# Kernel tuning notes

Measured on AMD Instinct MI355X. Metric: run time of the kernel, lower is better.

Reference implementation:

```python
import jax, jax.numpy as jnp
import numpy as np

# CaMoE_Block MoE dispatch/combine reference.
# Assumptions (undefined submodules in source): RWKV7_TimeMix/att residual omitted
# (h = ln2(x) directly); SparseRWKVFFN experts modeled as RWKV channel-mix FFNs
# y = relu(h @ W1)^2 @ W2; the LinearTransformerExpert (last expert) uses the same
# FFN form with recon_loss = 0; per-expert confidence head conf_e = sigmoid(h @ wc_e + bc_e).
# Faithful parts: winner selection, winning-bid lookup, straight-through scale
# factor conf / (stop_grad(conf) + 1e-6), per-expert compute, scatter-combine, residual.

B, T, C = 4, 2048, 1024
E = 5            # num_rwkv_experts + 1
H = 4 * C        # FFN hidden
LN_EPS = 1e-5


def setup_inputs() -> dict:
    key = jax.random.key(0)
    ks = jax.random.split(key, 8)
    x = jax.random.normal(ks[0], (B, T, C), dtype=jnp.float32)
    winners = jax.random.randint(ks[1], (B, T), 0, E)
    gamma = jnp.ones((C,), jnp.float32)
    beta = jnp.zeros((C,), jnp.float32)
    w1 = jax.random.normal(ks[2], (E, C, H), jnp.float32) * (1.0 / np.sqrt(C))
    w2 = jax.random.normal(ks[3], (E, H, C), jnp.float32) * (1.0 / np.sqrt(H))
    wc = jax.random.normal(ks[4], (E, C), jnp.float32) * (1.0 / np.sqrt(C))
    bc = jnp.zeros((E,), jnp.float32)
    return {"x": x, "winners": winners, "gamma": gamma, "beta": beta,
            "w1": w1, "w2": w2, "wc": wc, "bc": bc}


def _layernorm(x, gamma, beta):
    mu = jnp.mean(x, axis=-1, keepdims=True)
    var = jnp.mean(jnp.square(x - mu), axis=-1, keepdims=True)
    return (x - mu) * jax.lax.rsqrt(var + LN_EPS) * gamma + beta


def reference(x, winners, gamma, beta, w1, w2, wc, bc):
    b, t, c = x.shape
    e = w1.shape[0]
    h = _layernorm(x, gamma, beta)
    hf = h.reshape(-1, c)                     # [N, C]
    win = winners.reshape(-1)                 # [N]

    # per-expert confidences (bids)
    conf = jax.nn.sigmoid(hf @ wc.T + bc)     # [N, E]
    winning_bids = jnp.take_along_axis(conf, win[:, None], axis=1)  # [N, 1]
    scale = winning_bids / (jax.lax.stop_gradient(winning_bids) + 1e-6)

    # dense all-expert FFN (squared-ReLU channel mix), then top-1 select
    k = jnp.square(jax.nn.relu(jnp.einsum('nc,ech->enh', hf, w1)))  # [E, N, H]
    y = jnp.einsum('enh,ehc->enc', k, w2)                            # [E, N, C]
    sel = jax.nn.one_hot(win, e, dtype=y.dtype)                      # [N, E]
    expert_out = jnp.einsum('ne,enc->nc', sel, y)                    # scatter-combine

    out = (expert_out * scale).reshape(b, t, c)
    return x + out
```

## Files before the change

### kernel.cpp

```cpp
#include <hip/hip_runtime.h>
#include <hip/hip_bf16.h>
#include <stdint.h>

#define N_TOK 8192
#define C_DIM 1024
#define H_DIM 4096
#define E_NUM 5
#define LN_EPS 1e-5f
#define NT_MAX 69
#define N_PAD (NT_MAX * 128)

typedef __hip_bfloat16 bf16;
using s8v = __attribute__((ext_vector_type(8))) short;
using f4v = __attribute__((ext_vector_type(4))) float;

__device__ __forceinline__ void async_ld16(const bf16* g, bf16* l) {
    __builtin_amdgcn_global_load_lds(
        (const __attribute__((address_space(1))) void*)g,
        (__attribute__((address_space(3))) void*)l,
        16, 0, 0);
}

__global__ void init_meta_kernel(int* meta) {
    if (threadIdx.x < 16) meta[threadIdx.x] = 0;
}

__global__ __launch_bounds__(256) void count_kernel(
    const int* __restrict__ win, int* __restrict__ meta)
{
    __shared__ int c[E_NUM];
    if (threadIdx.x < E_NUM) c[threadIdx.x] = 0;
    __syncthreads();
    int n = blockIdx.x * 256 + threadIdx.x;
    atomicAdd(&c[win[n]], 1);
    __syncthreads();
    if (threadIdx.x < E_NUM) atomicAdd(&meta[threadIdx.x], c[threadIdx.x]);
}

__global__ void scan_kernel(int* meta) {
    if (threadIdx.x == 0) {
        int off = 0;
        for (int e = 0; e < E_NUM; ++e) {
            meta[5 + e] = off;
            off += (meta[e] + 127) & ~127;
            meta[11 + e] = 0;
        }
        meta[10] = off;
        int ti = 0;
        for (int e = 0; e < E_NUM; ++e) {
            int tiles = (meta[e] + 127) >> 7;
            for (int j = 0; j < tiles; ++j) meta[16 + ti++] = e;
        }
        for (; ti < NT_MAX; ++ti) meta[16 + ti] = -1;
    }
}

__global__ __launch_bounds__(256) void scatter_kernel(
    const int* __restrict__ win, int* __restrict__ meta,
    int* __restrict__ idx, int* __restrict__ pos)
{
    __shared__ int c[E_NUM];
    __shared__ int base[E_NUM];
    if (threadIdx.x < E_NUM) c[threadIdx.x] = 0;
    __syncthreads();
    int n = blockIdx.x * 256 + threadIdx.x;
    int e = win[n];
    int lr = atomicAdd(&c[e], 1);
    __syncthreads();
    if (threadIdx.x < E_NUM)
        base[threadIdx.x] = atomicAdd(&meta[11 + threadIdx.x], c[threadIdx.x]);
    __syncthreads();
    int p = meta[5 + e] + base[e] + lr;
    idx[p] = n;
    pos[n] = p;
}

__global__ __launch_bounds__(256) void ln_conf_kernel(
    const float* __restrict__ x, const int* __restrict__ win,
    const float* __restrict__ gamma, const float* __restrict__ beta,
    const float* __restrict__ wc, const float* __restrict__ bc,
    const int* __restrict__ pos,
    bf16* __restrict__ hbuf, float* __restrict__ scl)
{
    int n = blockIdx.x;
    int t = threadIdx.x;
    const float* xr = x + (size_t)n * C_DIM;
    float v[4];
    float s = 0.f, ss = 0.f;
#pragma unroll
    for (int i = 0; i < 4; ++i) {
        v[i] = xr[t + i * 256];
        s += v[i];
        ss += v[i] * v[i];
    }
#pragma unroll
    for (int off = 32; off > 0; off >>= 1) {
        s  += __shfl_down(s, off);
        ss += __shfl_down(ss, off);
    }
    __shared__ float red[8];
    __shared__ float mu_s, rv_s;
    int wave = t >> 6, lane = t & 63;
    if (lane == 0) { red[wave] = s; red[4 + wave] = ss; }
    __syncthreads();
    if (t == 0) {
        float S  = red[0] + red[1] + red[2] + red[3];
        float SS = red[4] + red[5] + red[6] + red[7];
        float mu = S * (1.f / C_DIM);
        float var = SS * (1.f / C_DIM) - mu * mu;
        mu_s = mu;
        rv_s = rsqrtf(var + LN_EPS);
    }
    __syncthreads();
    float mu = mu_s, rv = rv_s;
    int e = win[n];
    int p = pos[n];
    const float* wce = wc + (size_t)e * C_DIM;
    float dot = 0.f;
#pragma unroll
    for (int i = 0; i < 4; ++i) {
        int ci = t + i * 256;
        float hv = (v[i] - mu) * rv * gamma[ci] + beta[ci];
        hbuf[(size_t)p * C_DIM + ci] = (bf16)hv;
        dot += hv * wce[ci];
    }
#pragma unroll
    for (int off = 32; off > 0; off >>= 1) dot += __shfl_down(dot, off);
    if (lane == 0) red[wave] = dot;
    __syncthreads();
    if (t == 0) {
        float z = red[0] + red[1] + red[2] + red[3] + bc[e];
        float conf = 1.f / (1.f + expf(-z));
        scl[p] = conf / (conf + 1e-6f);
    }
}

__global__ __launch_bounds__(256) void transpose_cvt_kernel(
    const float* __restrict__ src, bf16* __restrict__ dst, int R, int S)
{
    __shared__ float tile[64][65];
    size_t ebase = (size_t)blockIdx.z * (size_t)R * (size_t)S;
    int s0 = blockIdx.x * 64;
    int r0 = blockIdx.y * 64;
    int t = threadIdx.x;
    int lr = t >> 4;
    int lc = (t & 15) * 4;
#pragma unroll
    for (int i = 0; i < 4; ++i) {
        int r = lr + i * 16;
        float4 v = *(const float4*)(src + ebase + (size_t)(r0 + r) * S + s0 + lc);
        tile[r][lc + 0] = v.x;
        tile[r][lc + 1] = v.y;
        tile[r][lc + 2] = v.z;
        tile[r][lc + 3] = v.w;
    }
    __syncthreads();
    int sc = t >> 2;
#pragma unroll
    for (int p = 0; p < 2; ++p) {
        int ch = (t & 3) + p * 4;
        bf16 vals[8];
#pragma unroll
        for (int j = 0; j < 8; ++j)
            vals[j] = (bf16)tile[ch * 8 + j][sc];
        *(s8v*)(dst + ebase + (size_t)(s0 + sc) * R + r0 + ch * 8) = *(s8v*)vals;
    }
}


__global__ __launch_bounds__(256) void gemm1_kernel(
    const bf16* __restrict__ hbuf, const bf16* __restrict__ w1t,
    const int* __restrict__ meta, bf16* __restrict__ ks)
{
    const int GX = H_DIM / 128;
    const int NWG = GX * NT_MAX;
    int d = blockIdx.y * GX + blockIdx.x;
    int w = (d & 7) * (NWG >> 3) + (d >> 3);
    int bx = w & (GX - 1);
    int ti = w / GX;
    int e = meta[16 + ti];
    if (e < 0) return;

    int base_p = meta[5 + e];
    int cnt = meta[e];
    int m0 = ti * 128 - base_p;
    int n0 = bx * 128;

    __shared__ __align__(16) bf16 As[128 * 32];
    __shared__ __align__(16) bf16 Bs[128 * 32];

    int t = threadIdx.x;
    int lane = t & 63;
    int wv = t >> 6;
    int wr = wv >> 1, wcol = wv & 1;

    int i0 = (t & 7) ^ ((t >> 3) & 7);
    int srow = 2 * (t >> 3) + (i0 >> 2);
    int schk = i0 & 3;

    int r1 = min(m0 + srow, cnt - 1);
    int r2 = min(m0 + 64 + srow, cnt - 1);
    const bf16* ga1 = hbuf + (size_t)(base_p + r1) * C_DIM + schk * 8;
    const bf16* ga2 = hbuf + (size_t)(base_p + r2) * C_DIM + schk * 8;
    const bf16* wbase = w1t + (size_t)e * H_DIM * C_DIM;
    const bf16* gb1 = wbase + (size_t)(n0 + srow) * C_DIM + schk * 8;
    const bf16* gb2 = wbase + (size_t)(n0 + 64 + srow) * C_DIM + schk * 8;

    bf16* la1 = As + t * 8;
    bf16* la2 = As + 2048 + t * 8;
    bf16* lb1 = Bs + t * 8;
    bf16* lb2 = Bs + 2048 + t * 8;

    int kq = lane >> 4;
    int rhalf = (lane & 15) >> 1;
    int ifrag = ((lane & 1) << 2) | kq;
    int foff = rhalf * 64 + (ifrag ^ rhalf) * 8;
    const bf16* Af = As + wr * 2048 + foff;
    const bf16* Bf = Bs + wcol * 2048 + foff;

    f4v acc[4][4];
    f4v zero = {0.f, 0.f, 0.f, 0.f};
#pragma unroll
    for (int i = 0; i < 4; ++i)
#pragma unroll
        for (int j = 0; j < 4; ++j) acc[i][j] = zero;

    for (int kb = 0; kb < C_DIM / 32; ++kb) {
        __syncthreads();
        async_ld16(ga1, la1); ga1 += 32;
        async_ld16(ga2, la2); ga2 += 32;
        async_ld16(gb1, lb1); gb1 += 32;
        async_ld16(gb2, lb2); gb2 += 32;
        __syncthreads();
        s8v af[4], bfv[4];
#pragma unroll
        for (int mi = 0; mi < 4; ++mi)
            af[mi] = *(const s8v*)(Af + mi * 512);
#pragma unroll
        for (int ni = 0; ni < 4; ++ni)
            bfv[ni] = *(const s8v*)(Bf + ni * 512);
#pragma unroll
        for (int mi = 0; mi < 4; ++mi)
#pragma unroll
            for (int ni = 0; ni < 4; ++ni)
                acc[mi][ni] = __builtin_amdgcn_mfma_f32_16x16x32_bf16(af[mi], bfv[ni], acc[mi][ni], 0, 0, 0);
    }

#pragma unroll
    for (int mi = 0; mi < 4; ++mi) {
#pragma unroll
        for (int r = 0; r < 4; ++r) {
            int row_local = wr * 64 + mi * 16 + ((lane >> 4) << 2) + r;
            int gm = m0 + row_local;
            if (gm < cnt) {
                size_t p = (size_t)(base_p + gm);
#pragma unroll
                for (int ni = 0; ni < 4; ++ni) {
                    int col = n0 + wcol * 64 + ni * 16 + (lane & 15);
                    float v = acc[mi][ni][r];
                    float rl = fmaxf(v, 0.f);
                    ks[p * H_DIM + col] = (bf16)(rl * rl);
                }
            }
        }
    }
}

__global__ __launch_bounds__(256) void gemm2_kernel(
    const bf16* __restrict__ ks, const bf16* __restrict__ w2t,
    const int* __restrict__ idx, const int* __restrict__ meta,
    const float* __restrict__ x, const float* __restrict__ scl,
    float* __restrict__ out)
{
    const int GX = C_DIM / 128;
    const int NWG = GX * NT_MAX;
    int d = blockIdx.y * GX + blockIdx.x;
    int w = (d & 7) * (NWG >> 3) + (d >> 3);
    int bx = w & (GX - 1);
    int ti = w / GX;
    int e = meta[16 + ti];
    if (e < 0) return;

    int base_p = meta[5 + e];
    int cnt = meta[e];
    int m0 = ti * 128 - base_p;
    int n0 = bx * 128;

    __shared__ __align__(16) bf16 As[3][128 * 32];
    __shared__ __align__(16) bf16 Bs[3][128 * 32];

    int t = threadIdx.x;
    int lane = t & 63;
    int wv = t >> 6;
    int wr = wv >> 1, wcol = wv & 1;

    int i0 = (t & 7) ^ ((t >> 3) & 7);
    int srow = 2 * (t >> 3) + (i0 >> 2);
    int schk = i0 & 3;

    int r1 = min(m0 + srow, cnt - 1);
    int r2 = min(m0 + 64 + srow, cnt - 1);
    const bf16* ga1 = ks + (size_t)(base_p + r1) * H_DIM + schk * 8;
    const bf16* ga2 = ks + (size_t)(base_p + r2) * H_DIM + schk * 8;
    const bf16* wbase = w2t + (size_t)e * C_DIM * H_DIM;
    const bf16* gb1 = wbase + (size_t)(n0 + srow) * H_DIM + schk * 8;
    const bf16* gb2 = wbase + (size_t)(n0 + 64 + srow) * H_DIM + schk * 8;

    int lo1 = t * 8;
    int lo2 = 2048 + t * 8;

    int kq = lane >> 4;
    int rhalf = (lane & 15) >> 1;
    int ifrag = ((lane & 1) << 2) | kq;
    int foff = rhalf * 64 + (ifrag ^ rhalf) * 8;
    int aoff = wr * 2048 + foff;
    int boff = wcol * 2048 + foff;

    f4v acc[4][4];
    f4v zero = {0.f, 0.f, 0.f, 0.f};
#pragma unroll
    for (int i = 0; i < 4; ++i)
#pragma unroll
        for (int j = 0; j < 4; ++j) acc[i][j] = zero;

    const int nk = H_DIM / 32;

#pragma unroll
    for (int pt = 0; pt < 2; ++pt) {
        async_ld16(ga1, &As[pt][lo1]); ga1 += 32;
        async_ld16(ga2, &As[pt][lo2]); ga2 += 32;
        async_ld16(gb1, &Bs[pt][lo1]); gb1 += 32;
        async_ld16(gb2, &Bs[pt][lo2]); gb2 += 32;
    }

    int cur = 0, st = 2;
    for (int kb = 0; kb < nk; ++kb) {
        if (kb < nk - 2) {
            async_ld16(ga1, &As[st][lo1]); ga1 += 32;
            async_ld16(ga2, &As[st][lo2]); ga2 += 32;
            async_ld16(gb1, &Bs[st][lo1]); gb1 += 32;
            async_ld16(gb2, &Bs[st][lo2]); gb2 += 32;
            asm volatile("s_waitcnt vmcnt(8)" ::: "memory");
        } else if (kb == nk - 2) {
            asm volatile("s_waitcnt vmcnt(4)" ::: "memory");
        } else {
            asm volatile("s_waitcnt vmcnt(0)" ::: "memory");
        }
        __builtin_amdgcn_s_barrier();

        const bf16* Ac = &As[cur][0];
        const bf16* Bc = &Bs[cur][0];
        s8v af[4], bfv[4];
#pragma unroll
        for (int mi = 0; mi < 4; ++mi)
            af[mi] = *(const s8v*)(Ac + aoff + mi * 512);
#pragma unroll
        for (int ni = 0; ni < 4; ++ni)
            bfv[ni] = *(const s8v*)(Bc + boff + ni * 512);
#pragma unroll
        for (int mi = 0; mi < 4; ++mi)
#pragma unroll
            for (int ni = 0; ni < 4; ++ni)
                acc[mi][ni] = __builtin_amdgcn_mfma_f32_16x16x32_bf16(af[mi], bfv[ni], acc[mi][ni], 0, 0, 0);

        asm volatile("s_waitcnt lgkmcnt(0)" ::: "memory");
        __builtin_amdgcn_s_barrier();
        cur = (cur == 2) ? 0 : cur + 1;
        st  = (st  == 2) ? 0 : st  + 1;
    }

#pragma unroll
    for (int mi = 0; mi < 4; ++mi) {
        int tok[4];
        float sclv[4];
#pragma unroll
        for (int r = 0; r < 4; ++r) {
            int row_local = wr * 64 + mi * 16 + ((lane >> 4) << 2) + r;
            int gm = m0 + row_local;
            if (gm < cnt) {
                tok[r] = idx[base_p + gm];
                sclv[r] = scl[base_p + gm];
            } else {
                tok[r] = -1;
                sclv[r] = 0.f;
            }
        }
#pragma unroll
        for (int ni = 0; ni < 4; ++ni) {
            int col = n0 + wcol * 64 + ni * 16 + (lane & 15);
#pragma unroll
            for (int r = 0; r < 4; ++r) {
                if (tok[r] >= 0) {
                    size_t o = (size_t)tok[r] * C_DIM + col;
                    out[o] = x[o] + acc[mi][ni][r] * sclv[r];
                }
            }
        }
    }
}

extern "C" void kernel_launch(void* const* d_in, const int* in_sizes, int n_in,
                              void* d_out, int out_size, void* d_ws, size_t ws_size,
                              hipStream_t stream) {
    const float* x     = (const float*)d_in[0];
    const int*   win   = (const int*)d_in[1];
    const float* gamma = (const float*)d_in[2];
    const float* beta  = (const float*)d_in[3];
    const float* w1    = (const float*)d_in[4];
    const float* w2    = (const float*)d_in[5];
    const float* wc    = (const float*)d_in[6];
    const float* bc    = (const float*)d_in[7];
    float* out = (float*)d_out;

    char* ws = (char*)d_ws;
    size_t o = 0;
    bf16* w1t  = (bf16*)(ws + o); o += (size_t)E_NUM * H_DIM * C_DIM * 2;
    bf16* w2t  = (bf16*)(ws + o); o += (size_t)E_NUM * C_DIM * H_DIM * 2;
    bf16* hbuf = (bf16*)(ws + o); o += (size_t)N_PAD * C_DIM * 2;
    bf16* ks   = (bf16*)(ws + o); o += (size_t)N_PAD * H_DIM * 2;
    float* scl = (float*)(ws + o); o += (size_t)N_PAD * 4;
    int* idx   = (int*)(ws + o);   o += (size_t)N_PAD * 4;
    int* pos   = (int*)(ws + o);   o += (size_t)N_TOK * 4;
    int* meta  = (int*)(ws + o);   o += 512;

    hipLaunchKernelGGL(init_meta_kernel, dim3(1), dim3(64), 0, stream, meta);
    hipLaunchKernelGGL(count_kernel, dim3(N_TOK / 256), dim3(256), 0, stream, win, meta);
    hipLaunchKernelGGL(scan_kernel, dim3(1), dim3(64), 0, stream, meta);
    hipLaunchKernelGGL(scatter_kernel, dim3(N_TOK / 256), dim3(256), 0, stream, win, meta, idx, pos);
    hipLaunchKernelGGL(transpose_cvt_kernel, dim3(H_DIM / 64, C_DIM / 64, E_NUM), dim3(256), 0, stream,
                       w1, w1t, C_DIM, H_DIM);
    hipLaunchKernelGGL(transpose_cvt_kernel, dim3(C_DIM / 64, H_DIM / 64, E_NUM), dim3(256), 0, stream,
                       w2, w2t, H_DIM, C_DIM);
    hipLaunchKernelGGL(ln_conf_kernel, dim3(N_TOK), dim3(256), 0, stream,
                       x, win, gamma, beta, wc, bc, pos, hbuf, scl);
    hipLaunchKernelGGL(gemm1_kernel, dim3(H_DIM / 128, NT_MAX), dim3(256), 0, stream,
                       hbuf, w1t, meta, ks);
    hipLaunchKernelGGL(gemm2_kernel, dim3(C_DIM / 128, NT_MAX), dim3(256), 0, stream,
                       ks, w2t, idx, meta, x, scl, out);
}
```

Baseline: 443.7 us.

## Pipeline gemm1 with triple-buffered async loads and deepen gemm2 to four stages

The first expert GEMM drops its single-buffer load/sync loop and uses the same triple-buffered async global-to-LDS pipeline as the second GEMM, with vmcnt-based waits. The second GEMM goes from three to four stages, keeping more loads in flight. Both kernels raise wave priority around the MFMA block, and the transpose kernel changes its write-thread mapping so that consecutive threads write adjacent 16-byte chunks of one row. The cost is more LDS per workgroup, which may reduce occupancy.

```diff
diff --git a/kernel.cpp b/kernel.cpp
--- a/kernel.cpp
+++ b/kernel.cpp
@@ -155,10 +155,11 @@
         tile[r][lc + 3] = v.w;
     }
     __syncthreads();
-    int sc = t >> 2;
+    int ch = t & 7;
+    int scb = t >> 3;
 #pragma unroll
     for (int p = 0; p < 2; ++p) {
-        int ch = (t & 3) + p * 4;
+        int sc = scb + p * 32;
         bf16 vals[8];
 #pragma unroll
         for (int j = 0; j < 8; ++j)
@@ -186,8 +187,8 @@
     int m0 = ti * 128 - base_p;
     int n0 = bx * 128;
 
-    __shared__ __align__(16) bf16 As[128 * 32];
-    __shared__ __align__(16) bf16 Bs[128 * 32];
+    __shared__ __align__(16) bf16 As[3][128 * 32];
+    __shared__ __align__(16) bf16 Bs[3][128 * 32];
 
     int t = threadIdx.x;
     int lane = t & 63;
@@ -206,106 +207,6 @@
     const bf16* gb1 = wbase + (size_t)(n0 + srow) * C_DIM + schk * 8;
     const bf16* gb2 = wbase + (size_t)(n0 + 64 + srow) * C_DIM + schk * 8;
 
-    bf16* la1 = As + t * 8;
-    bf16* la2 = As + 2048 + t * 8;
-    bf16* lb1 = Bs + t * 8;
-    bf16* lb2 = Bs + 2048 + t * 8;
-
-    int kq = lane >> 4;
-    int rhalf = (lane & 15) >> 1;
-    int ifrag = ((lane & 1) << 2) | kq;
-    int foff = rhalf * 64 + (ifrag ^ rhalf) * 8;
-    const bf16* Af = As + wr * 2048 + foff;
-    const bf16* Bf = Bs + wcol * 2048 + foff;
-
-    f4v acc[4][4];
-    f4v zero = {0.f, 0.f, 0.f, 0.f};
-#pragma unroll
-    for (int i = 0; i < 4; ++i)
-#pragma unroll
-        for (int j = 0; j < 4; ++j) acc[i][j] = zero;
-
-    for (int kb = 0; kb < C_DIM / 32; ++kb) {
-        __syncthreads();
-        async_ld16(ga1, la1); ga1 += 32;
-        async_ld16(ga2, la2); ga2 += 32;
-        async_ld16(gb1, lb1); gb1 += 32;
-        async_ld16(gb2, lb2); gb2 += 32;
-        __syncthreads();
-        s8v af[4], bfv[4];
-#pragma unroll
-        for (int mi = 0; mi < 4; ++mi)
-            af[mi] = *(const s8v*)(Af + mi * 512);
-#pragma unroll
-        for (int ni = 0; ni < 4; ++ni)
-            bfv[ni] = *(const s8v*)(Bf + ni * 512);
-#pragma unroll
-        for (int mi = 0; mi < 4; ++mi)
-#pragma unroll
-            for (int ni = 0; ni < 4; ++ni)
-                acc[mi][ni] = __builtin_amdgcn_mfma_f32_16x16x32_bf16(af[mi], bfv[ni], acc[mi][ni], 0, 0, 0);
-    }
-
-#pragma unroll
-    for (int mi = 0; mi < 4; ++mi) {
-#pragma unroll
-        for (int r = 0; r < 4; ++r) {
-            int row_local = wr * 64 + mi * 16 + ((lane >> 4) << 2) + r;
-            int gm = m0 + row_local;
-            if (gm < cnt) {
-                size_t p = (size_t)(base_p + gm);
-#pragma unroll
-                for (int ni = 0; ni < 4; ++ni) {
-                    int col = n0 + wcol * 64 + ni * 16 + (lane & 15);
-                    float v = acc[mi][ni][r];
-                    float rl = fmaxf(v, 0.f);
-                    ks[p * H_DIM + col] = (bf16)(rl * rl);
-                }
-            }
-        }
-    }
-}
-
-__global__ __launch_bounds__(256) void gemm2_kernel(
-    const bf16* __restrict__ ks, const bf16* __restrict__ w2t,
-    const int* __restrict__ idx, const int* __restrict__ meta,
-    const float* __restrict__ x, const float* __restrict__ scl,
-    float* __restrict__ out)
-{
-    const int GX = C_DIM / 128;
-    const int NWG = GX * NT_MAX;
-    int d = blockIdx.y * GX + blockIdx.x;
-    int w = (d & 7) * (NWG >> 3) + (d >> 3);
-    int bx = w & (GX - 1);
-    int ti = w / GX;
-    int e = meta[16 + ti];
-    if (e < 0) return;
-
-    int base_p = meta[5 + e];
-    int cnt = meta[e];
-    int m0 = ti * 128 - base_p;
-    int n0 = bx * 128;
-
-    __shared__ __align__(16) bf16 As[3][128 * 32];
-    __shared__ __align__(16) bf16 Bs[3][128 * 32];
-
-    int t = threadIdx.x;
-    int lane = t & 63;
-    int wv = t >> 6;
-    int wr = wv >> 1, wcol = wv & 1;
-
-    int i0 = (t & 7) ^ ((t >> 3) & 7);
-    int srow = 2 * (t >> 3) + (i0 >> 2);
-    int schk = i0 & 3;
-
-    int r1 = min(m0 + srow, cnt - 1);
-    int r2 = min(m0 + 64 + srow, cnt - 1);
-    const bf16* ga1 = ks + (size_t)(base_p + r1) * H_DIM + schk * 8;
-    const bf16* ga2 = ks + (size_t)(base_p + r2) * H_DIM + schk * 8;
-    const bf16* wbase = w2t + (size_t)e * C_DIM * H_DIM;
-    const bf16* gb1 = wbase + (size_t)(n0 + srow) * H_DIM + schk * 8;
-    const bf16* gb2 = wbase + (size_t)(n0 + 64 + srow) * H_DIM + schk * 8;
-
     int lo1 = t * 8;
     int lo2 = 2048 + t * 8;
 
@@ -323,7 +224,7 @@
 #pragma unroll
         for (int j = 0; j < 4; ++j) acc[i][j] = zero;
 
-    const int nk = H_DIM / 32;
+    const int nk = C_DIM / 32;
 
 #pragma unroll
     for (int pt = 0; pt < 2; ++pt) {
@@ -357,16 +258,145 @@
 #pragma unroll
         for (int ni = 0; ni < 4; ++ni)
             bfv[ni] = *(const s8v*)(Bc + boff + ni * 512);
+        __builtin_amdgcn_s_setprio(1);
 #pragma unroll
         for (int mi = 0; mi < 4; ++mi)
 #pragma unroll
             for (int ni = 0; ni < 4; ++ni)
                 acc[mi][ni] = __builtin_amdgcn_mfma_f32_16x16x32_bf16(af[mi], bfv[ni], acc[mi][ni], 0, 0, 0);
+        __builtin_amdgcn_s_setprio(0);
 
         asm volatile("s_waitcnt lgkmcnt(0)" ::: "memory");
         __builtin_amdgcn_s_barrier();
         cur = (cur == 2) ? 0 : cur + 1;
         st  = (st  == 2) ? 0 : st  + 1;
+    }
+
+#pragma unroll
+    for (int mi = 0; mi < 4; ++mi) {
+#pragma unroll
+        for (int r = 0; r < 4; ++r) {
+            int row_local = wr * 64 + mi * 16 + ((lane >> 4) << 2) + r;
+            int gm = m0 + row_local;
+            if (gm < cnt) {
+                size_t p = (size_t)(base_p + gm);
+#pragma unroll
+                for (int ni = 0; ni < 4; ++ni) {
+                    int col = n0 + wcol * 64 + ni * 16 + (lane & 15);
+                    float v = acc[mi][ni][r];
+                    float rl = fmaxf(v, 0.f);
+                    ks[p * H_DIM + col] = (bf16)(rl * rl);
+                }
+            }
+        }
+    }
+}
+
+__global__ __launch_bounds__(256) void gemm2_kernel(
+    const bf16* __restrict__ ks, const bf16* __restrict__ w2t,
+    const int* __restrict__ idx, const int* __restrict__ meta,
+    const float* __restrict__ x, const float* __restrict__ scl,
+    float* __restrict__ out)
+{
+    const int GX = C_DIM / 128;
+    const int NWG = GX * NT_MAX;
+    int d = blockIdx.y * GX + blockIdx.x;
+    int w = (d & 7) * (NWG >> 3) + (d >> 3);
+    int bx = w & (GX - 1);
+    int ti = w / GX;
+    int e = meta[16 + ti];
+    if (e < 0) return;
+
+    int base_p = meta[5 + e];
+    int cnt = meta[e];
+    int m0 = ti * 128 - base_p;
+    int n0 = bx * 128;
+
+    __shared__ __align__(16) bf16 As[4][128 * 32];
+    __shared__ __align__(16) bf16 Bs[4][128 * 32];
+
+    int t = threadIdx.x;
+    int lane = t & 63;
+    int wv = t >> 6;
+    int wr = wv >> 1, wcol = wv & 1;
+
+    int i0 = (t & 7) ^ ((t >> 3) & 7);
+    int srow = 2 * (t >> 3) + (i0 >> 2);
+    int schk = i0 & 3;
+
+    int r1 = min(m0 + srow, cnt - 1);
+    int r2 = min(m0 + 64 + srow, cnt - 1);
+    const bf16* ga1 = ks + (size_t)(base_p + r1) * H_DIM + schk * 8;
+    const bf16* ga2 = ks + (size_t)(base_p + r2) * H_DIM + schk * 8;
+    const bf16* wbase = w2t + (size_t)e * C_DIM * H_DIM;
+    const bf16* gb1 = wbase + (size_t)(n0 + srow) * H_DIM + schk * 8;
+    const bf16* gb2 = wbase + (size_t)(n0 + 64 + srow) * H_DIM + schk * 8;
+
+    int lo1 = t * 8;
+    int lo2 = 2048 + t * 8;
+
+    int kq = lane >> 4;
+    int rhalf = (lane & 15) >> 1;
+    int ifrag = ((lane & 1) << 2) | kq;
+    int foff = rhalf * 64 + (ifrag ^ rhalf) * 8;
+    int aoff = wr * 2048 + foff;
+    int boff = wcol * 2048 + foff;
+
+    f4v acc[4][4];
+    f4v zero = {0.f, 0.f, 0.f, 0.f};
+#pragma unroll
+    for (int i = 0; i < 4; ++i)
+#pragma unroll
+        for (int j = 0; j < 4; ++j) acc[i][j] = zero;
+
+    const int nk = H_DIM / 32;
+
+#pragma unroll
+    for (int pt = 0; pt < 3; ++pt) {
+        async_ld16(ga1, &As[pt][lo1]); ga1 += 32;
+        async_ld16(ga2, &As[pt][lo2]); ga2 += 32;
+        async_ld16(gb1, &Bs[pt][lo1]); gb1 += 32;
+        async_ld16(gb2, &Bs[pt][lo2]); gb2 += 32;
+    }
+
+    int cur = 0, st = 3;
+    for (int kb = 0; kb < nk; ++kb) {
+        if (kb < nk - 3) {
+            async_ld16(ga1, &As[st][lo1]); ga1 += 32;
+            async_ld16(ga2, &As[st][lo2]); ga2 += 32;
+            async_ld16(gb1, &Bs[st][lo1]); gb1 += 32;
+            async_ld16(gb2, &Bs[st][lo2]); gb2 += 32;
+            asm volatile("s_waitcnt vmcnt(12)" ::: "memory");
+        } else if (kb == nk - 3) {
+            asm volatile("s_waitcnt vmcnt(8)" ::: "memory");
+        } else if (kb == nk - 2) {
+            asm volatile("s_waitcnt vmcnt(4)" ::: "memory");
+        } else {
+            asm volatile("s_waitcnt vmcnt(0)" ::: "memory");
+        }
+        __builtin_amdgcn_s_barrier();
+
+        const bf16* Ac = &As[cur][0];
+        const bf16* Bc = &Bs[cur][0];
+        s8v af[4], bfv[4];
+#pragma unroll
+        for (int mi = 0; mi < 4; ++mi)
+            af[mi] = *(const s8v*)(Ac + aoff + mi * 512);
+#pragma unroll
+        for (int ni = 0; ni < 4; ++ni)
+            bfv[ni] = *(const s8v*)(Bc + boff + ni * 512);
+        __builtin_amdgcn_s_setprio(1);
+#pragma unroll
+        for (int mi = 0; mi < 4; ++mi)
+#pragma unroll
+            for (int ni = 0; ni < 4; ++ni)
+                acc[mi][ni] = __builtin_amdgcn_mfma_f32_16x16x32_bf16(af[mi], bfv[ni], acc[mi][ni], 0, 0, 0);
+        __builtin_amdgcn_s_setprio(0);
+
+        asm volatile("s_waitcnt lgkmcnt(0)" ::: "memory");
+        __builtin_amdgcn_s_barrier();
+        cur = (cur + 1) & 3;
+        st  = (st  + 1) & 3;
     }
 
 #pragma unroll
```

Measured after the change: 528.0 us. +19.0%, slower.
